# Kernel tuning notes

Hardware: AMD Instinct MI355X
Metric: run time of the kernel (lower is better)

The kernel has to match this reference:

```python
import jax, jax.numpy as jnp
import numpy as np

B, S, D, H, HD, NF, NL, V = 16, 2048, 768, 12, 64, 32, 12, 2362
EPS = 1e-6  # fast_transformers LinearAttention eps


def _rope_tables(seq_len, dim):
    inv_freq = 1.0 / (10000.0 ** (jnp.arange(0, dim, 2, dtype=jnp.float32) / dim))
    t = jnp.arange(seq_len, dtype=jnp.float32)
    freqs = jnp.einsum('s,f->sf', t, inv_freq)
    emb = jnp.concatenate([freqs, freqs], axis=-1)[None, :, None, :]  # [1,S,1,HD]
    return jnp.cos(emb), jnp.sin(emb)


def _rot_half(x):
    x1, x2 = jnp.split(x, 2, axis=-1)
    return jnp.concatenate([-x2, x1], axis=-1)


def _ln(x, g, b):
    m = jnp.mean(x, axis=-1, keepdims=True)
    v = jnp.var(x, axis=-1, keepdims=True)
    return (x - m) / jnp.sqrt(v + 1e-5) * g + b


def setup_inputs():
    key = jax.random.key(0)
    ks = jax.random.split(key, 16)
    w = lambda k, shape: jax.random.normal(k, shape, jnp.float32) * 0.02
    return {
        'idx': jax.random.randint(ks[0], (B, S), 0, V),
        'mask': jnp.ones((B, S), jnp.int32),
        'emb': w(ks[1], (V, D)),
        'wq': w(ks[2], (NL, D, D)), 'bq': jnp.zeros((NL, D), jnp.float32),
        'wk': w(ks[3], (NL, D, D)), 'bk': jnp.zeros((NL, D), jnp.float32),
        'wv': w(ks[4], (NL, D, D)), 'bv': jnp.zeros((NL, D), jnp.float32),
        'wo': w(ks[5], (NL, D, D)), 'bo': jnp.zeros((NL, D), jnp.float32),
        'omega': jax.random.normal(ks[6], (NL, HD, NF), jnp.float32),
        'g1': jnp.ones((NL, D), jnp.float32), 'be1': jnp.zeros((NL, D), jnp.float32),
        'w1': w(ks[7], (NL, D, D)), 'c1': jnp.zeros((NL, D), jnp.float32),
        'w2': w(ks[8], (NL, D, D)), 'c2': jnp.zeros((NL, D), jnp.float32),
        'g2': jnp.ones((NL, D), jnp.float32), 'be2': jnp.zeros((NL, D), jnp.float32),
        'gf': jnp.ones((D,), jnp.float32), 'bf': jnp.zeros((D,), jnp.float32),
    }


def reference(idx, mask, emb, wq, bq, wk, bk, wv, bv, wo, bo, omega,
              g1, be1, w1, c1, w2, c2, g2, be2, gf, bf):
    x = emb[idx]                     # token embedding [B,S,D]; dropout = identity (eval)
    m = mask.astype(x.dtype)         # LengthMask from mask.sum(-1); mask is contiguous ones
    cos, sin = _rope_tables(S, HD)
    for l in range(NL):
        q = (x @ wq[l] + bq[l]).reshape(B, S, H, HD)
        k = (x @ wk[l] + bk[l]).reshape(B, S, H, HD)
        v = (x @ wv[l] + bv[l]).reshape(B, S, H, HD)
        q = q * cos + _rot_half(q) * sin
        k = k * cos + _rot_half(k) * sin
        # GeneralizedRandomFeatures: phi(x) = relu(x @ omega)
        Qf = jax.nn.relu(jnp.einsum('bshd,df->bshf', q, omega[l]))
        Kf = jax.nn.relu(jnp.einsum('bshd,df->bshf', k, omega[l])) * m[:, :, None, None]
        KV = jnp.einsum('bshf,bshd->bhfd', Kf, v)                       # [B,H,NF,HD]
        Z = 1.0 / (jnp.einsum('bshf,bhf->bsh', Qf, Kf.sum(axis=1)) + EPS)
        a = jnp.einsum('bshf,bhfd,bsh->bshd', Qf, KV, Z).reshape(B, S, D)
        x = x + (a @ wo[l] + bo[l])           # residual (dropout=identity)
        x = _ln(x, g1[l], be1[l])             # post-norm
        y = jax.nn.gelu(x @ w1[l] + c1[l], approximate=False) @ w2[l] + c2[l]
        x = _ln(x + y, g2[l], be2[l])
    return _ln(x, gf, bf)                     # final encoder LayerNorm
```

## Files before the change

kernel.cpp:

```cpp
#include <hip/hip_runtime.h>
#include <cstdint>
#include <cstddef>

typedef __bf16 bf16;
typedef __bf16 bf16x8 __attribute__((ext_vector_type(8)));
typedef __bf16 bf16x4 __attribute__((ext_vector_type(4)));
typedef float f32x4 __attribute__((ext_vector_type(4)));

#define NB 16
#define SS 2048
#define HH 12
#define NLL 12
#define MTOK (NB*SS)

#define BARRIER() do { asm volatile("" ::: "memory"); __builtin_amdgcn_s_barrier(); asm volatile("" ::: "memory"); } while (0)
#define VMCNT0()  asm volatile("s_waitcnt vmcnt(0)" ::: "memory")

__device__ __forceinline__ void load16_lds(const bf16* g, bf16* l) {
    __builtin_amdgcn_global_load_lds((const __attribute__((address_space(1))) void*)g,
                                     (__attribute__((address_space(3))) void*)l, 16, 0, 0);
}

__global__ void diag_k(float* out, float code) {
    if (threadIdx.x == 0 && blockIdx.x == 0) out[0] = code;
}

__global__ __launch_bounds__(256) void packw_k(const float* __restrict__ wq, const float* __restrict__ wk,
                                               const float* __restrict__ wv, const float* __restrict__ wo,
                                               const float* __restrict__ w1, const float* __restrict__ w2,
                                               int l, bf16* qkvT_l, bf16* oT_l, bf16* w1T_l, bf16* w2T_l) {
    __shared__ float tile[32][33];
    int which = blockIdx.z;
    const float* srcs[6] = {wq, wk, wv, wo, w1, w2};
    const float* src = srcs[which] + (size_t)l * 589824;
    bf16* dst;
    if (which < 3)       dst = qkvT_l + (size_t)which * 589824;
    else if (which == 3) dst = oT_l;
    else if (which == 4) dst = w1T_l;
    else                 dst = w2T_l;
    int tx = threadIdx.x, ty = threadIdx.y;
    int bx = blockIdx.x, by = blockIdx.y;
#pragma unroll
    for (int j = 0; j < 4; ++j)
        tile[ty + j*8][tx] = src[(size_t)(by*32 + ty + j*8) * 768 + bx*32 + tx];
    __syncthreads();
#pragma unroll
    for (int j = 0; j < 4; ++j)
        dst[(size_t)(bx*32 + ty + j*8) * 768 + by*32 + tx] = (bf16)tile[tx][ty + j*8];
}

__global__ void packb_k(const float* __restrict__ bq, const float* __restrict__ bk,
                        const float* __restrict__ bv, float* bqkv) {
    int i = blockIdx.x * 256 + threadIdx.x;
    if (i >= NLL * 2304) return;
    int l = i / 2304, c = i % 2304;
    float v = (c < 768) ? bq[l*768 + c] : (c < 1536) ? bk[l*768 + c - 768] : bv[l*768 + c - 1536];
    bqkv[i] = v;
}

__global__ void rope_k(float* cosT, float* sinT) {
    int i = blockIdx.x * 256 + threadIdx.x;
    int s = i >> 6, j = i & 63, f = j & 31;
    float inv = powf(10000.f, -(float)(2*f) * (1.0f/64.0f));
    float ang = (float)s * inv;
    cosT[i] = cosf(ang);
    sinT[i] = sinf(ang);
}

__global__ __launch_bounds__(192) void embed_k(const int* __restrict__ idx, const float* __restrict__ emb,
                                               float* __restrict__ x, bf16* __restrict__ xb) {
    size_t tok = blockIdx.x;
    int t = threadIdx.x;
    int id = idx[tok];
    float4 v = *(const float4*)&emb[(size_t)id * 768 + t*4];
    *(float4*)&x[tok * 768 + t*4] = v;
    bf16x4 o; o[0] = (bf16)v.x; o[1] = (bf16)v.y; o[2] = (bf16)v.z; o[3] = (bf16)v.w;
    *(bf16x4*)&xb[tok * 768 + t*4] = o;
}

template <int MODE>
__global__ __launch_bounds__(512, 2)
void gemm256_k(const bf16* __restrict__ A, const bf16* __restrict__ Bt,
               const float* __restrict__ bias, float* resout, bf16* outb, int N) {
    const int K = 768;
    __shared__ bf16 As[2][16384];
    __shared__ bf16 Bs[2][16384];
    const int t = threadIdx.x;
    const int w = t >> 6, lane = t & 63;
    const int wr = w >> 2, wc = w & 3;

    const int nx = gridDim.x;
    const int L = blockIdx.y * nx + blockIdx.x;
    const int xcd = L & 7, bi = L >> 3;
    const int bcol = (bi % nx) * 256;
    const int brow = ((bi / nx) * 8 + xcd) * 256;

    const int srow0 = t >> 3;
    const int scb   = (t & 7) * 16;
    const int scbs  = scb ^ ((srow0 & 7) << 4);
    const int scol  = scbs >> 1;

    auto stageA = [&](int s, int k0, int hh) {
        const bf16* g0 = A + (size_t)(brow + hh*128 + srow0)      * K + k0 + scol;
        const bf16* g1 = A + (size_t)(brow + hh*128 + srow0 + 64) * K + k0 + scol;
        load16_lds(g0, &As[s][hh*8192 + t*8]);
        load16_lds(g1, &As[s][hh*8192 + t*8 + 4096]);
    };
    auto stageB = [&](int s, int k0, int hh) {
        const bf16* g0 = Bt + (size_t)(bcol + hh*128 + srow0)      * K + k0 + scol;
        const bf16* g1 = Bt + (size_t)(bcol + hh*128 + srow0 + 64) * K + k0 + scol;
        load16_lds(g0, &Bs[s][hh*8192 + t*8]);
        load16_lds(g1, &Bs[s][hh*8192 + t*8 + 4096]);
    };

    const int rowa = lane & 15, kg = lane >> 4;
    const int rsw  = (rowa & 7) << 4;

    f32x4  acc[8][4] = {};
    bf16x8 af[4][2];
    bf16x8 bg[2][2][2];

#define LOADAF(CUR, MH)                                                          \
    _Pragma("unroll") for (int mi2 = 0; mi2 < 4; ++mi2)                          \
    _Pragma("unroll") for (int ks = 0; ks < 2; ++ks) {                           \
        int lrow = wr*128 + (MH)*64 + mi2*16 + rowa;                             \
        int cbyt = (ks*64 + kg*16) ^ rsw;                                        \
        af[mi2][ks] = *(const bf16x8*)&As[CUR][lrow*64 + (cbyt >> 1)];           \
    }
#define LOADBG(CUR, NH)                                                          \
    _Pragma("unroll") for (int ni2 = 0; ni2 < 2; ++ni2)                          \
    _Pragma("unroll") for (int ks = 0; ks < 2; ++ks) {                           \
        int lrow = wc*64 + (NH)*32 + ni2*16 + rowa;                              \
        int cbyt = (ks*64 + kg*16) ^ rsw;                                        \
        bg[NH][ni2][ks] = *(const bf16x8*)&Bs[CUR][lrow*64 + (cbyt >> 1)];       \
    }
#define MFMAQ(MH, NH)                                                            \
    __builtin_amdgcn_s_setprio(1);                                               \
    _Pragma("unroll") for (int mi2 = 0; mi2 < 4; ++mi2)                          \
    _Pragma("unroll") for (int ni2 = 0; ni2 < 2; ++ni2)                          \
    _Pragma("unroll") for (int ks = 0; ks < 2; ++ks)                             \
        acc[(MH)*4+mi2][(NH)*2+ni2] = __builtin_amdgcn_mfma_f32_16x16x32_bf16(   \
            af[mi2][ks], bg[NH][ni2][ks], acc[(MH)*4+mi2][(NH)*2+ni2], 0, 0, 0); \
    __builtin_amdgcn_s_setprio(0);

    stageA(0, 0, 0); stageA(0, 0, 1); stageB(0, 0, 0); stageB(0, 0, 1);
    VMCNT0();
    BARRIER();

    for (int kt = 0; kt < 12; ++kt) {
        const int cur = kt & 1, nb = cur ^ 1;
        const int kn = (kt + 1) * 64;
        const bool st = (kt < 11);
        LOADAF(cur, 0);
        LOADBG(cur, 0);
        if (st) { stageA(nb, kn, 0); stageA(nb, kn, 1); }
        BARRIER();
        MFMAQ(0, 0);
        BARRIER();
        LOADBG(cur, 1);
        if (st) stageB(nb, kn, 0);
        BARRIER();
        MFMAQ(0, 1);
        BARRIER();
        LOADAF(cur, 1);
        if (st) stageB(nb, kn, 1);
        BARRIER();
        MFMAQ(1, 1);
        BARRIER();
        MFMAQ(1, 0);
        VMCNT0();
        BARRIER();
    }
#undef LOADAF
#undef LOADBG
#undef MFMAQ

    const int r0 = (lane >> 4) * 4, c0 = lane & 15;
#pragma unroll
    for (int mi = 0; mi < 8; ++mi) {
#pragma unroll
        for (int ni = 0; ni < 4; ++ni) {
            int col = bcol + wc * 64 + ni * 16 + c0;
            float bv = bias[col];
#pragma unroll
            for (int r = 0; r < 4; ++r) {
                int row = brow + wr * 128 + mi * 16 + r0 + r;
                float v = acc[mi][ni][r] + bv;
                size_t o = (size_t)row * N + col;
                if (MODE == 0) outb[o] = (bf16)v;
                else if (MODE == 1) outb[o] = (bf16)(0.5f * v * (1.f + erff(v * 0.70710678118f)));
                else resout[o] = v + resout[o];
            }
        }
    }
}

__global__ __launch_bounds__(192) void phi_k(const bf16* __restrict__ qkv, const float* __restrict__ cosT,
                                             const float* __restrict__ sinT, const float* __restrict__ omega_l,
                                             const int* __restrict__ mask, bf16* __restrict__ Qf,
                                             bf16* __restrict__ Kf) {
    __shared__ float roped[2][4][12][65];
    __shared__ float om[64][32];
    int t = threadIdx.x;
    size_t tok0 = (size_t)blockIdx.x * 4;

    for (int i = t; i < 2048; i += 192) ((float*)om)[i] = omega_l[i];

    {
        int side = t / 96, cr = t % 96, h = cr >> 3, cq = cr & 7;
        float sgn = (cq < 4) ? -1.f : 1.f;
        for (int it = 0; it < 4; ++it) {
            size_t tokg = tok0 + it;
            int s = (int)(tokg & (SS - 1));
            const bf16* rowp = qkv + tokg * 2304 + side * 768 + h * 64;
            bf16x8 mv = *(const bf16x8*)(rowp + cq * 8);
            bf16x8 pv = *(const bf16x8*)(rowp + (cq ^ 4) * 8);
            const float* cp = cosT + s * 64 + cq * 8;
            const float* sp = sinT + s * 64 + cq * 8;
#pragma unroll
            for (int e = 0; e < 8; ++e) {
                float r = (float)mv[e] * cp[e] + sgn * (float)pv[e] * sp[e];
                roped[side][it][h][cq * 8 + e] = r;
            }
        }
    }
    __syncthreads();

    int side = t / 96, rr = t % 96, h = rr >> 3, f0 = (rr & 7) * 4;
    float acc[4][4] = {};
    for (int d = 0; d < 64; ++d) {
        float4 o = *(const float4*)&om[d][f0];
#pragma unroll
        for (int tk = 0; tk < 4; ++tk) {
            float qv = roped[side][tk][h][d];
            acc[tk][0] += qv * o.x; acc[tk][1] += qv * o.y;
            acc[tk][2] += qv * o.z; acc[tk][3] += qv * o.w;
        }
    }
    bf16* outb = (side == 0) ? Qf : Kf;
#pragma unroll
    for (int tk = 0; tk < 4; ++tk) {
        size_t tokg = tok0 + tk;
        float m = (side == 1) ? (float)mask[tokg] : 1.f;
        bf16x4 v;
        v[0] = (bf16)(fmaxf(acc[tk][0], 0.f) * m);
        v[1] = (bf16)(fmaxf(acc[tk][1], 0.f) * m);
        v[2] = (bf16)(fmaxf(acc[tk][2], 0.f) * m);
        v[3] = (bf16)(fmaxf(acc[tk][3], 0.f) * m);
        *(bf16x4*)&outb[(tokg * 12 + h) * 32 + f0] = v;
    }
}

__global__ __launch_bounds__(256) void kvp_k(const bf16* __restrict__ Kf, const bf16* __restrict__ qkv,
                                             float* __restrict__ KVp, float* __restrict__ Ksp) {
    int ch = blockIdx.x, h = blockIdx.y, b = blockIdx.z;
    __shared__ float kts[64][32];
    __shared__ bf16 vts[64][64];
    int t = threadIdx.x;
    int fg = t & 15, dg = t >> 4;
    int f0 = fg * 2, d0 = dg * 4;
    float acc[8] = {};
    float ksm[2] = {};
    for (int s0 = ch * 256; s0 < ch * 256 + 256; s0 += 64) {
        __syncthreads();
        {
            int row = t >> 2, slot = t & 3;
            bf16x8 k8 = *(const bf16x8*)&Kf[((size_t)(b * SS + s0 + row) * 12 + h) * 32 + slot * 8];
#pragma unroll
            for (int e = 0; e < 8; ++e) kts[row][slot * 8 + e] = (float)k8[e];
            int c0 = t, c1 = t + 256;
            *(float4*)&vts[c0 >> 3][(c0 & 7) * 8] =
                *(const float4*)&qkv[(size_t)(b * SS + s0 + (c0 >> 3)) * 2304 + 1536 + h * 64 + (c0 & 7) * 8];
            *(float4*)&vts[c1 >> 3][(c1 & 7) * 8] =
                *(const float4*)&qkv[(size_t)(b * SS + s0 + (c1 >> 3)) * 2304 + 1536 + h * 64 + (c1 & 7) * 8];
        }
        __syncthreads();
        for (int sl = 0; sl < 64; ++sl) {
            float k0 = kts[sl][f0], k1 = kts[sl][f0 + 1];
            float v0 = (float)vts[sl][d0 + 0], v1 = (float)vts[sl][d0 + 1];
            float v2 = (float)vts[sl][d0 + 2], v3 = (float)vts[sl][d0 + 3];
            acc[0] += k0 * v0; acc[1] += k0 * v1; acc[2] += k0 * v2; acc[3] += k0 * v3;
            acc[4] += k1 * v0; acc[5] += k1 * v1; acc[6] += k1 * v2; acc[7] += k1 * v3;
            if (dg == 0) { ksm[0] += k0; ksm[1] += k1; }
        }
    }
    size_t base = (((size_t)(b * 12 + h) * 8 + ch) * 32) * 64;
#pragma unroll
    for (int i = 0; i < 2; ++i)
#pragma unroll
        for (int j = 0; j < 4; ++j)
            KVp[base + (size_t)(f0 + i) * 64 + d0 + j] = acc[i * 4 + j];
    if (dg == 0) {
        size_t kb = ((size_t)(b * 12 + h) * 8 + ch) * 32;
        Ksp[kb + f0] = ksm[0]; Ksp[kb + f0 + 1] = ksm[1];
    }
}

__global__ __launch_bounds__(256) void kvc_k(const float* __restrict__ KVp, const float* __restrict__ Ksp,
                                             float* __restrict__ KV, float* __restrict__ Ksum) {
    int bh = blockIdx.x, t = threadIdx.x;
    size_t base = (size_t)bh * 8 * 2048;
    float v[8] = {};
    for (int ch = 0; ch < 8; ++ch)
#pragma unroll
        for (int j = 0; j < 8; ++j) v[j] += KVp[base + (size_t)ch * 2048 + t * 8 + j];
#pragma unroll
    for (int j = 0; j < 8; ++j) KV[(size_t)bh * 2048 + t * 8 + j] = v[j];
    if (t < 32) {
        float s = 0.f;
        for (int ch = 0; ch < 8; ++ch) s += Ksp[((size_t)bh * 8 + ch) * 32 + t];
        Ksum[(size_t)bh * 32 + t] = s;
    }
}

__global__ __launch_bounds__(256) void comb_k(const bf16* __restrict__ Qf, const float* __restrict__ KV,
                                              const float* __restrict__ Ksum, bf16* __restrict__ aout) {
    int ch = blockIdx.x, h = blockIdx.y, b = blockIdx.z;
    int bh = b * 12 + h;
    __shared__ float kvs[32][64];
    __shared__ float ks[32];
    int t = threadIdx.x;
    {
        const float* kvsrc = KV + (size_t)bh * 2048;
#pragma unroll
        for (int j = 0; j < 8; ++j) ((float*)kvs)[t + j * 256] = kvsrc[t + j * 256];
    }
    if (t < 32) ks[t] = Ksum[(size_t)bh * 32 + t];
    __syncthreads();
    int sl = t >> 6, d = t & 63;
    for (int g = 0; g < 16; ++g) {
        int s = ch * 64 + g * 4 + sl;
        size_t tok = (size_t)b * SS + s;
        const bf16* qf = Qf + (tok * 12 + h) * 32;
        float accd = 0.f, accz = 0.f;
#pragma unroll
        for (int f = 0; f < 32; ++f) {
            float q = (float)qf[f];
            accd += q * kvs[f][d];
            accz += q * ks[f];
        }
        float z = 1.f / (accz + 1e-6f);
        aout[tok * 768 + h * 64 + d] = (bf16)(accd * z);
    }
}

__global__ __launch_bounds__(192) void ln_k(const float* src, const float* __restrict__ g,
                                            const float* __restrict__ be, float* xout,
                                            bf16* xbout) {
    size_t tok = blockIdx.x;
    int t = threadIdx.x;
    float4 v = *(const float4*)&src[tok * 768 + t * 4];
    float s = v.x + v.y + v.z + v.w;
    float q = v.x * v.x + v.y * v.y + v.z * v.z + v.w * v.w;
#pragma unroll
    for (int off = 32; off > 0; off >>= 1) { s += __shfl_down(s, off); q += __shfl_down(q, off); }
    __shared__ float sred[3], qred[3];
    int w = t >> 6, lane = t & 63;
    if (lane == 0) { sred[w] = s; qred[w] = q; }
    __syncthreads();
    s = sred[0] + sred[1] + sred[2];
    q = qred[0] + qred[1] + qred[2];
    float mean = s * (1.f / 768.f);
    float var = q * (1.f / 768.f) - mean * mean;
    float inv = rsqrtf(var + 1e-5f);
    float4 gg = *(const float4*)&g[t * 4];
    float4 bb = *(const float4*)&be[t * 4];
    float4 o;
    o.x = (v.x - mean) * inv * gg.x + bb.x;
    o.y = (v.y - mean) * inv * gg.y + bb.y;
    o.z = (v.z - mean) * inv * gg.z + bb.z;
    o.w = (v.w - mean) * inv * gg.w + bb.w;
    *(float4*)&xout[tok * 768 + t * 4] = o;
    if (xbout) {
        bf16x4 ob; ob[0] = (bf16)o.x; ob[1] = (bf16)o.y; ob[2] = (bf16)o.z; ob[3] = (bf16)o.w;
        *(bf16x4*)&xbout[tok * 768 + t * 4] = ob;
    }
}

extern "C" void kernel_launch(void* const* d_in, const int* in_sizes, int n_in,
                              void* d_out, int out_size, void* d_ws, size_t ws_size,
                              hipStream_t stream) {
    const int*   idx   = (const int*)d_in[0];
    const int*   mask  = (const int*)d_in[1];
    const float* emb   = (const float*)d_in[2];
    const float* wq    = (const float*)d_in[3];
    const float* bq    = (const float*)d_in[4];
    const float* wk    = (const float*)d_in[5];
    const float* bk    = (const float*)d_in[6];
    const float* wv    = (const float*)d_in[7];
    const float* bv    = (const float*)d_in[8];
    const float* wo    = (const float*)d_in[9];
    const float* bo    = (const float*)d_in[10];
    const float* omega = (const float*)d_in[11];
    const float* g1    = (const float*)d_in[12];
    const float* be1   = (const float*)d_in[13];
    const float* w1    = (const float*)d_in[14];
    const float* c1    = (const float*)d_in[15];
    const float* w2    = (const float*)d_in[16];
    const float* c2    = (const float*)d_in[17];
    const float* g2    = (const float*)d_in[18];
    const float* be2   = (const float*)d_in[19];
    const float* gf    = (const float*)d_in[20];
    const float* bff   = (const float*)d_in[21];
    float* dout = (float*)d_out;

    char* wsb = (char*)d_ws;
    size_t off = 0;
    auto nxt = [&](size_t bytes) -> void* {
        void* p = wsb + off;
        off += bytes;
        off = (off + 255) & ~(size_t)255;
        return p;
    };

    float* cosT  = (float*)nxt((size_t)SS * 64 * 4);
    float* sinT  = (float*)nxt((size_t)SS * 64 * 4);
    bf16*  qkvTl = (bf16*)nxt((size_t)2304 * 768 * 2);
    bf16*  oTl   = (bf16*)nxt((size_t)768 * 768 * 2);
    bf16*  w1Tl  = (bf16*)nxt((size_t)768 * 768 * 2);
    bf16*  w2Tl  = (bf16*)nxt((size_t)768 * 768 * 2);
    float* bqkv  = (float*)nxt((size_t)NLL * 2304 * 4);
    float* x     = (float*)nxt((size_t)MTOK * 768 * 4);
    bf16*  xb    = (bf16*)nxt((size_t)MTOK * 768 * 2);
    bf16*  qkv   = (bf16*)nxt((size_t)MTOK * 2304 * 2);
    bf16*  Qf    = (bf16*)nxt((size_t)MTOK * 384 * 2);
    bf16*  Kf    = (bf16*)nxt((size_t)MTOK * 384 * 2);
    float* KVp   = (float*)nxt((size_t)NB * HH * 8 * 2048 * 4);
    float* Ksp   = (float*)nxt((size_t)NB * HH * 8 * 32 * 4);
    float* KV    = (float*)nxt((size_t)NB * HH * 2048 * 4);
    float* Ksum  = (float*)nxt((size_t)NB * HH * 32 * 4);
    size_t needed = off;

    if (ws_size < needed) {
        diag_k<<<dim3(1), dim3(64), 0, stream>>>(dout, 10000.f + (float)(ws_size >> 20));
        return;
    }

    bf16* abuf = qkv;
    bf16* h1   = (bf16*)((char*)qkv + (size_t)MTOK * 768 * 2);

    packb_k<<<dim3((NLL * 2304 + 255) / 256), dim3(256), 0, stream>>>(bq, bk, bv, bqkv);
    rope_k<<<dim3(SS * 64 / 256), dim3(256), 0, stream>>>(cosT, sinT);
    embed_k<<<dim3(MTOK), dim3(192), 0, stream>>>(idx, emb, x, xb);

    for (int l = 0; l < NLL; ++l) {
        const float* bqkv_l = bqkv + (size_t)l * 2304;
        const float* om_l   = omega + (size_t)l * 2048;

        packw_k<<<dim3(24, 24, 6), dim3(32, 8), 0, stream>>>(wq, wk, wv, wo, w1, w2, l, qkvTl, oTl, w1Tl, w2Tl);
        gemm256_k<0><<<dim3(9, 128), dim3(512), 0, stream>>>(xb, qkvTl, bqkv_l, nullptr, qkv, 2304);
        phi_k<<<dim3(MTOK / 4), dim3(192), 0, stream>>>(qkv, cosT, sinT, om_l, mask, Qf, Kf);
        kvp_k<<<dim3(8, HH, NB), dim3(256), 0, stream>>>(Kf, qkv, KVp, Ksp);
        kvc_k<<<dim3(NB * HH), dim3(256), 0, stream>>>(KVp, Ksp, KV, Ksum);
        comb_k<<<dim3(32, HH, NB), dim3(256), 0, stream>>>(Qf, KV, Ksum, abuf);
        gemm256_k<2><<<dim3(3, 128), dim3(512), 0, stream>>>(abuf, oTl, bo + (size_t)l * 768, x, nullptr, 768);
        ln_k<<<dim3(MTOK), dim3(192), 0, stream>>>(x, g1 + (size_t)l * 768, be1 + (size_t)l * 768, x, xb);
        gemm256_k<1><<<dim3(3, 128), dim3(512), 0, stream>>>(xb, w1Tl, c1 + (size_t)l * 768, nullptr, h1, 768);
        gemm256_k<2><<<dim3(3, 128), dim3(512), 0, stream>>>(h1, w2Tl, c2 + (size_t)l * 768, x, nullptr, 768);
        ln_k<<<dim3(MTOK), dim3(192), 0, stream>>>(x, g2 + (size_t)l * 768, be2 + (size_t)l * 768, x, xb);
    }
    ln_k<<<dim3(MTOK), dim3(192), 0, stream>>>(x, gf, bff, dout, nullptr);
}
```

Before: 8.918 ms.

## Use 128x128 GEMM tiles for N=768 projections and vectorize attention helper kernels

Adds a 128x128-tile, 256-thread GEMM and uses it for the output projection and both MLP GEMMs, raising the block count from 384 to 1536 so all CUs get work with less tail imbalance. The kvp kernel now reads K and V from LDS with vector loads and unrolls its loop. The comb kernel keeps its KV column and Ksum in registers instead of LDS and reads Qf as 8-wide vectors. In exchange, the smaller tiles give less operand reuse per block, and the register-held arrays raise register pressure.

```diff
diff --git a/kernel.cpp b/kernel.cpp
--- a/kernel.cpp
+++ b/kernel.cpp
@@ -195,6 +195,78 @@
     }
 }
 
+template <int MODE>
+__global__ __launch_bounds__(256)
+void gemm128_k(const bf16* __restrict__ A, const bf16* __restrict__ Bt,
+               const float* __restrict__ bias, float* resout, bf16* outb, int N) {
+    const int K = 768;
+    __shared__ bf16 As[128 * 64];
+    __shared__ bf16 Bs[128 * 64];
+    const int t = threadIdx.x;
+    const int w = t >> 6, lane = t & 63;
+    const int wr = w >> 1, wc = w & 1;
+
+    const int nx = gridDim.x;
+    const int L = blockIdx.y * nx + blockIdx.x;
+    const int xcd = L & 7, bi = L >> 3;
+    const int bcol = (bi % nx) * 128;
+    const int brow = ((bi / nx) * 8 + xcd) * 128;
+
+    const int srow = t >> 3;
+    const int scol = (((t & 7) * 16) ^ ((srow & 7) << 4)) >> 1;
+    const int rowa = lane & 15, kg = lane >> 4;
+    const int rsw  = (rowa & 7) << 4;
+
+    f32x4 acc[4][4] = {};
+
+    for (int k0 = 0; k0 < K; k0 += 64) {
+        __syncthreads();
+#pragma unroll
+        for (int j = 0; j < 4; ++j) {
+            load16_lds(A  + (size_t)(brow + j*32 + srow) * K + k0 + scol, &As[j*2048 + t*8]);
+            load16_lds(Bt + (size_t)(bcol + j*32 + srow) * K + k0 + scol, &Bs[j*2048 + t*8]);
+        }
+        __syncthreads();
+        bf16x8 af[4][2], bg[4][2];
+#pragma unroll
+        for (int mi = 0; mi < 4; ++mi)
+#pragma unroll
+            for (int ks = 0; ks < 2; ++ks)
+                af[mi][ks] = *(const bf16x8*)&As[(wr*64 + mi*16 + rowa)*64 + (((ks*64 + kg*16) ^ rsw) >> 1)];
+#pragma unroll
+        for (int ni = 0; ni < 4; ++ni)
+#pragma unroll
+            for (int ks = 0; ks < 2; ++ks)
+                bg[ni][ks] = *(const bf16x8*)&Bs[(wc*64 + ni*16 + rowa)*64 + (((ks*64 + kg*16) ^ rsw) >> 1)];
+#pragma unroll
+        for (int mi = 0; mi < 4; ++mi)
+#pragma unroll
+            for (int ni = 0; ni < 4; ++ni)
+#pragma unroll
+                for (int ks = 0; ks < 2; ++ks)
+                    acc[mi][ni] = __builtin_amdgcn_mfma_f32_16x16x32_bf16(af[mi][ks], bg[ni][ks], acc[mi][ni], 0, 0, 0);
+    }
+
+    const int r0 = (lane >> 4) * 4, c0 = lane & 15;
+#pragma unroll
+    for (int mi = 0; mi < 4; ++mi) {
+#pragma unroll
+        for (int ni = 0; ni < 4; ++ni) {
+            int col = bcol + wc * 64 + ni * 16 + c0;
+            float bv = bias[col];
+#pragma unroll
+            for (int r = 0; r < 4; ++r) {
+                int row = brow + wr * 64 + mi * 16 + r0 + r;
+                float v = acc[mi][ni][r] + bv;
+                size_t o = (size_t)row * N + col;
+                if (MODE == 0) outb[o] = (bf16)v;
+                else if (MODE == 1) outb[o] = (bf16)(0.5f * v * (1.f + erff(v * 0.70710678118f)));
+                else resout[o] = v + resout[o];
+            }
+        }
+    }
+}
+
 __global__ __launch_bounds__(192) void phi_k(const bf16* __restrict__ qkv, const float* __restrict__ cosT,
                                              const float* __restrict__ sinT, const float* __restrict__ omega_l,
                                              const int* __restrict__ mask, bf16* __restrict__ Qf,
@@ -275,13 +347,14 @@
                 *(const float4*)&qkv[(size_t)(b * SS + s0 + (c1 >> 3)) * 2304 + 1536 + h * 64 + (c1 & 7) * 8];
         }
         __syncthreads();
+#pragma unroll 4
         for (int sl = 0; sl < 64; ++sl) {
-            float k0 = kts[sl][f0], k1 = kts[sl][f0 + 1];
-            float v0 = (float)vts[sl][d0 + 0], v1 = (float)vts[sl][d0 + 1];
-            float v2 = (float)vts[sl][d0 + 2], v3 = (float)vts[sl][d0 + 3];
-            acc[0] += k0 * v0; acc[1] += k0 * v1; acc[2] += k0 * v2; acc[3] += k0 * v3;
-            acc[4] += k1 * v0; acc[5] += k1 * v1; acc[6] += k1 * v2; acc[7] += k1 * v3;
-            if (dg == 0) { ksm[0] += k0; ksm[1] += k1; }
+            float2 kk = *(const float2*)&kts[sl][f0];
+            bf16x4 vv = *(const bf16x4*)&vts[sl][d0];
+            float v0 = (float)vv[0], v1 = (float)vv[1], v2 = (float)vv[2], v3 = (float)vv[3];
+            acc[0] += kk.x * v0; acc[1] += kk.x * v1; acc[2] += kk.x * v2; acc[3] += kk.x * v3;
+            acc[4] += kk.y * v0; acc[5] += kk.y * v1; acc[6] += kk.y * v2; acc[7] += kk.y * v3;
+            if (dg == 0) { ksm[0] += kk.x; ksm[1] += kk.y; }
         }
     }
     size_t base = (((size_t)(b * 12 + h) * 8 + ch) * 32) * 64;
@@ -317,27 +390,28 @@
                                               const float* __restrict__ Ksum, bf16* __restrict__ aout) {
     int ch = blockIdx.x, h = blockIdx.y, b = blockIdx.z;
     int bh = b * 12 + h;
-    __shared__ float kvs[32][64];
-    __shared__ float ks[32];
-    int t = threadIdx.x;
-    {
-        const float* kvsrc = KV + (size_t)bh * 2048;
-#pragma unroll
-        for (int j = 0; j < 8; ++j) ((float*)kvs)[t + j * 256] = kvsrc[t + j * 256];
-    }
-    if (t < 32) ks[t] = Ksum[(size_t)bh * 32 + t];
-    __syncthreads();
-    int sl = t >> 6, d = t & 63;
+    int t = threadIdx.x, sl = t >> 6, d = t & 63;
+    const float* kvb = KV + (size_t)bh * 2048;
+    const float* ksb = Ksum + (size_t)bh * 32;
+    float kvcol[32], ksr[32];
+#pragma unroll
+    for (int f = 0; f < 32; ++f) kvcol[f] = kvb[f * 64 + d];
+#pragma unroll
+    for (int f = 0; f < 32; ++f) ksr[f] = ksb[f];
     for (int g = 0; g < 16; ++g) {
         int s = ch * 64 + g * 4 + sl;
         size_t tok = (size_t)b * SS + s;
         const bf16* qf = Qf + (tok * 12 + h) * 32;
         float accd = 0.f, accz = 0.f;
 #pragma unroll
-        for (int f = 0; f < 32; ++f) {
-            float q = (float)qf[f];
-            accd += q * kvs[f][d];
-            accz += q * ks[f];
+        for (int fb = 0; fb < 4; ++fb) {
+            bf16x8 q8 = *(const bf16x8*)(qf + fb * 8);
+#pragma unroll
+            for (int e = 0; e < 8; ++e) {
+                float q = (float)q8[e];
+                accd += q * kvcol[fb * 8 + e];
+                accz += q * ksr[fb * 8 + e];
+            }
         }
         float z = 1.f / (accz + 1e-6f);
         aout[tok * 768 + h * 64 + d] = (bf16)(accd * z);
@@ -453,10 +527,10 @@
         kvp_k<<<dim3(8, HH, NB), dim3(256), 0, stream>>>(Kf, qkv, KVp, Ksp);
         kvc_k<<<dim3(NB * HH), dim3(256), 0, stream>>>(KVp, Ksp, KV, Ksum);
         comb_k<<<dim3(32, HH, NB), dim3(256), 0, stream>>>(Qf, KV, Ksum, abuf);
-        gemm256_k<2><<<dim3(3, 128), dim3(512), 0, stream>>>(abuf, oTl, bo + (size_t)l * 768, x, nullptr, 768);
+        gemm128_k<2><<<dim3(6, 256), dim3(256), 0, stream>>>(abuf, oTl, bo + (size_t)l * 768, x, nullptr, 768);
         ln_k<<<dim3(MTOK), dim3(192), 0, stream>>>(x, g1 + (size_t)l * 768, be1 + (size_t)l * 768, x, xb);
-        gemm256_k<1><<<dim3(3, 128), dim3(512), 0, stream>>>(xb, w1Tl, c1 + (size_t)l * 768, nullptr, h1, 768);
-        gemm256_k<2><<<dim3(3, 128), dim3(512), 0, stream>>>(h1, w2Tl, c2 + (size_t)l * 768, x, nullptr, 768);
+        gemm128_k<1><<<dim3(6, 256), dim3(256), 0, stream>>>(xb, w1Tl, c1 + (size_t)l * 768, nullptr, h1, 768);
+        gemm128_k<2><<<dim3(6, 256), dim3(256), 0, stream>>>(h1, w2Tl, c2 + (size_t)l * 768, x, nullptr, 768);
         ln_k<<<dim3(MTOK), dim3(192), 0, stream>>>(x, g2 + (size_t)l * 768, be2 + (size_t)l * 768, x, xb);
     }
     ln_k<<<dim3(MTOK), dim3(192), 0, stream>>>(x, gf, bff, dout, nullptr);
```

Result: faster. 8.535 ms (-4.3%).
